# Performance work log

Measured on AMD Instinct MI355X. Metric: run time of the kernel, lower is better.

Reference implementation:

```python
import jax, jax.numpy as jnp
import numpy as np

NUM_HEADS = 16
ROPE_BASE = 10000.0


def _rope_interleaved(x, cos, sin):
    # x: [B,S,H,Hd]; cos/sin: [S,Hd/2]. Interleaved pairs (even, odd).
    x1 = x[..., 0::2]
    x2 = x[..., 1::2]
    c = cos[None, :, None, :]
    s = sin[None, :, None, :]
    o1 = x1 * c - x2 * s
    o2 = x1 * s + x2 * c
    return jnp.stack([o1, o2], axis=-1).reshape(x.shape)


def setup_inputs() -> dict:
    key = jax.random.key(0)
    ks = jax.random.split(key, 5)
    B, S, D = 2, 2048, 2048
    init_scale = 0.02
    x = jax.random.normal(ks[0], (B, S, D), jnp.float32)
    Wq = jax.random.normal(ks[1], (D, D), jnp.float32) * init_scale
    Wk = jax.random.normal(ks[2], (D, D), jnp.float32) * init_scale
    Wv = jax.random.normal(ks[3], (D, D), jnp.float32) * init_scale
    Wo = jax.random.normal(ks[4], (D, D), jnp.float32) * init_scale
    return {"x": x, "Wq": Wq, "Wk": Wk, "Wv": Wv, "Wo": Wo}


def reference(x, Wq, Wk, Wv, Wo):
    B, S, D = x.shape
    H = NUM_HEADS
    Hd = D // H
    # QKV projections (bias-free)
    q = (x @ Wq).reshape(B, S, H, Hd)
    k = (x @ Wk).reshape(B, S, H, Hd)
    v = (x @ Wv).reshape(B, S, H, Hd)
    # Rotary embedding, interleaved, base 10000, full head_dim
    pos = jnp.arange(S, dtype=jnp.float32)
    inv_freq = 1.0 / (ROPE_BASE ** (jnp.arange(0, Hd, 2, dtype=jnp.float32) / Hd))
    angles = pos[:, None] * inv_freq[None, :]  # [S, Hd/2]
    cos, sin = jnp.cos(angles), jnp.sin(angles)
    q = _rope_interleaved(q, cos, sin)
    k = _rope_interleaved(k, cos, sin)
    # Causal scaled-dot-product attention (flash_attn_func default scale = Hd**-0.5)
    scale = Hd ** -0.5
    scores = jnp.einsum('bqhd,bkhd->bhqk', q, k) * scale
    causal = jnp.tril(jnp.ones((S, S), dtype=bool))
    scores = jnp.where(causal[None, None], scores, jnp.finfo(scores.dtype).min)
    probs = jax.nn.softmax(scores, axis=-1)
    attn = jnp.einsum('bhqk,bkhd->bqhd', probs, v).reshape(B, S, D)
    return attn @ Wo
```

## Files before the change

### kernel.cpp

```cpp
#include <hip/hip_runtime.h>
#include <hip/hip_bf16.h>

static constexpr int BB = 2;
static constexpr int SS = 2048;
static constexpr int DD = 2048;
static constexpr int HH = 16;
static constexpr int HD = 128;

typedef __bf16 bf16_t;
typedef __bf16 bf16x8 __attribute__((ext_vector_type(8)));
typedef __bf16 bf16x4 __attribute__((ext_vector_type(4)));
typedef float  floatx4 __attribute__((ext_vector_type(4)));

__device__ __forceinline__ void gl2lds16(const bf16_t* g, bf16_t* l) {
    __builtin_amdgcn_global_load_lds(
        (const __attribute__((address_space(1))) void*)g,
        (__attribute__((address_space(3))) void*)l, 16, 0, 0);
}

__global__ void cast_x_kernel(const float* __restrict__ x, bf16_t* __restrict__ xb) {
    int i = blockIdx.x * 256 + threadIdx.x;
    float4 v = ((const float4*)x)[i];
    bf16x4 o;
    o.x = (bf16_t)v.x; o.y = (bf16_t)v.y; o.z = (bf16_t)v.z; o.w = (bf16_t)v.w;
    ((bf16x4*)xb)[i] = o;
}

__global__ void transpose_cast_kernel(const float* __restrict__ W, bf16_t* __restrict__ Wt) {
    __shared__ float tile[32][33];
    int bx = blockIdx.x * 32;
    int by = blockIdx.y * 32;
    int tx = threadIdx.x, ty = threadIdx.y;
#pragma unroll
    for (int j = 0; j < 4; ++j)
        tile[ty + j * 8][tx] = W[(size_t)(by + ty + j * 8) * DD + bx + tx];
    __syncthreads();
#pragma unroll
    for (int j = 0; j < 4; ++j)
        Wt[(size_t)(bx + ty + j * 8) * DD + by + tx] = (bf16_t)tile[tx][ty + j * 8];
}

template <int MODE>
__global__ __launch_bounds__(256, 2) void gemm_bt_kernel(
    const bf16_t* __restrict__ A, const bf16_t* __restrict__ Bt,
    float* __restrict__ Cf, bf16_t* __restrict__ Qw, bf16_t* __restrict__ Kw,
    bf16_t* __restrict__ Vw, int N, int K) {
    __shared__ __align__(16) bf16_t As[128 * 64];
    __shared__ __align__(16) bf16_t Bs[128 * 64];

    const int t = threadIdx.x;
    const int lane = t & 63;
    const int wave = t >> 6;
    const int lrow = lane & 15;
    const int lkq  = lane >> 4;
    const int wm = (wave & 1) * 64;
    const int wn = (wave >> 1) * 64;
    const int m0 = blockIdx.y * 128;
    const int n0 = blockIdx.x * 128;

    floatx4 acc[4][4];
#pragma unroll
    for (int i = 0; i < 4; ++i)
#pragma unroll
        for (int j = 0; j < 4; ++j) acc[i][j] = (floatx4)0.0f;

    const int srow  = lane >> 3;
    const int sch   = (lane & 7) ^ srow;

    for (int k0 = 0; k0 < K; k0 += 64) {
        __syncthreads();
#pragma unroll
        for (int p = 0; p < 4; ++p) {
            int r = wave * 32 + p * 8 + srow;
            gl2lds16(A  + (size_t)(m0 + r) * K + k0 + sch * 8, As + (wave * 32 + p * 8) * 64);
            gl2lds16(Bt + (size_t)(n0 + r) * K + k0 + sch * 8, Bs + (wave * 32 + p * 8) * 64);
        }
        __syncthreads();
#pragma unroll
        for (int ks = 0; ks < 2; ++ks) {
            bf16x8 af[4], bg[4];
#pragma unroll
            for (int i = 0; i < 4; ++i) {
                int pos = ((ks * 4 + lkq) ^ (lrow & 7)) * 8;
                af[i] = *(const bf16x8*)(As + (wm + i * 16 + lrow) * 64 + pos);
                bg[i] = *(const bf16x8*)(Bs + (wn + i * 16 + lrow) * 64 + pos);
            }
#pragma unroll
            for (int i = 0; i < 4; ++i)
#pragma unroll
                for (int j = 0; j < 4; ++j)
                    acc[i][j] = __builtin_amdgcn_mfma_f32_16x16x32_bf16(af[i], bg[j], acc[i][j], 0, 0, 0);
        }
    }

#pragma unroll
    for (int i = 0; i < 4; ++i)
#pragma unroll
        for (int j = 0; j < 4; ++j)
#pragma unroll
            for (int r = 0; r < 4; ++r) {
                int m = m0 + wm + i * 16 + lkq * 4 + r;
                int n = n0 + wn + j * 16 + lrow;
                float v = acc[i][j][r];
                if (MODE == 1) {
                    Cf[(size_t)m * N + n] = v;
                } else {
                    bf16_t bv = (bf16_t)v;
                    int b = m >> 11, s = m & (SS - 1);
                    int nn = n & (DD - 1);
                    int h = nn >> 7, d = nn & 127;
                    size_t off = (((size_t)b * HH + h) * SS + s) * HD + d;
                    if (n < DD)            Qw[off] = bv;
                    else if (n < 2 * DD)   Kw[off] = bv;
                    else                   Vw[off] = bv;
                }
            }
}

__global__ void rope_kernel(bf16_t* __restrict__ Qw, bf16_t* __restrict__ Kw) {
    int idx = blockIdx.x * 256 + threadIdx.x;
    int i  = idx & 63;
    int s  = (idx >> 6) & (SS - 1);
    int bh = idx >> 17;
    float inv = expf(-(float)(2 * i) * (9.210340371976184f / 128.0f));
    float ang = (float)s * inv;
    float c = cosf(ang), sn = sinf(ang);
    size_t base = ((size_t)bh * SS + s) * HD + 2 * i;
    float q1 = (float)Qw[base], q2 = (float)Qw[base + 1];
    Qw[base]     = (bf16_t)(q1 * c - q2 * sn);
    Qw[base + 1] = (bf16_t)(q1 * sn + q2 * c);
    float k1 = (float)Kw[base], k2 = (float)Kw[base + 1];
    Kw[base]     = (bf16_t)(k1 * c - k2 * sn);
    Kw[base + 1] = (bf16_t)(k1 * sn + k2 * c);
}

__global__ void vtrans_kernel(const bf16_t* __restrict__ Vw, bf16_t* __restrict__ Vt) {
    __shared__ unsigned short lds[64][65];
    const int t = threadIdx.x;
    const int s0 = blockIdx.x * 64, d0 = blockIdx.y * 64, bh = blockIdx.z;
    const bf16_t* src = Vw + ((size_t)bh * SS + s0) * HD + d0;
    bf16_t* dst = Vt + ((size_t)bh * HD + d0) * SS + s0;
#pragma unroll
    for (int p = 0; p < 2; ++p) {
        int c = p * 256 + t;
        int s = c >> 3, ch = c & 7;
        uint4 v = *(const uint4*)(src + (size_t)s * HD + ch * 8);
        const unsigned short* pv = (const unsigned short*)&v;
#pragma unroll
        for (int e = 0; e < 8; ++e) lds[ch * 8 + e][s] = pv[e];
    }
    __syncthreads();
    {
        int d = t >> 2, sb = (t & 3) * 16;
        uint4 o[2];
        unsigned short* po = (unsigned short*)o;
#pragma unroll
        for (int e = 0; e < 16; ++e) po[e] = lds[d][sb + e];
        *(uint4*)(dst + (size_t)d * SS + sb) = o[0];
        *(uint4*)(dst + (size_t)d * SS + sb + 8) = o[1];
    }
}

__global__ __launch_bounds__(256, 2) void flash_attn_kernel(
    const bf16_t* __restrict__ Qw, const bf16_t* __restrict__ Kw,
    const bf16_t* __restrict__ Vtw, bf16_t* __restrict__ Attn) {
    __shared__ __align__(16) bf16_t Ks[64 * 128];
    __shared__ __align__(16) bf16_t Vs[128 * 64];
    __shared__ __align__(16) bf16_t Ps[4][16 * 72];

    const int t = threadIdx.x;
    const int lane = t & 63;
    const int wave = t >> 6;
    const int lrow = lane & 15;
    const int lkq  = lane >> 4;
    const int bx = blockIdx.x;
    const int qtile = (bx & 1) ? (bx >> 1) : (15 - (bx >> 1));
    const int bh = blockIdx.y;
    const int q0 = qtile * 128;

    const bf16_t* Qbh = Qw + (size_t)bh * SS * HD;
    const bf16_t* Kbh = Kw + (size_t)bh * SS * HD;
    const bf16_t* Vbh = Vtw + (size_t)bh * HD * SS;

    const int qb[2] = { q0 + wave * 16, q0 + 64 + wave * 16 };

    const float qscale = 0.08838834764831845f * 1.4426950408889634f;
    bf16x8 qf[2][4];
#pragma unroll
    for (int qs = 0; qs < 2; ++qs)
#pragma unroll
        for (int kc4 = 0; kc4 < 4; ++kc4) {
            qf[qs][kc4] = *(const bf16x8*)(Qbh + (size_t)(qb[qs] + lrow) * HD + kc4 * 32 + lkq * 8);
#pragma unroll
            for (int e = 0; e < 8; ++e) qf[qs][kc4][e] = (bf16_t)((float)qf[qs][kc4][e] * qscale);
        }

    floatx4 oacc[2][8];
#pragma unroll
    for (int qs = 0; qs < 2; ++qs)
#pragma unroll
        for (int i = 0; i < 8; ++i) oacc[qs][i] = (floatx4)0.0f;
    float m_i[2] = { -1e30f, -1e30f };
    float l_i[2] = { 0.0f, 0.0f };

    const int nch = 2 * qtile + 2;
    for (int kc = 0; kc < nch; ++kc) {
        __syncthreads();
#pragma unroll
        for (int p = 0; p < 4; ++p) {
            int row = wave * 16 + p * 4 + (lane >> 4);
            int gch = (lane & 15) ^ (row & 7);
            gl2lds16(Kbh + (size_t)(kc * 64 + row) * HD + gch * 8,
                     Ks + (wave * 16 + p * 4) * 128);
        }
#pragma unroll
        for (int p = 0; p < 4; ++p) {
            int row = wave * 32 + p * 8 + (lane >> 3);
            int gch = (lane & 7) ^ (row & 7);
            gl2lds16(Vbh + (size_t)row * SS + kc * 64 + gch * 8,
                     Vs + (wave * 32 + p * 8) * 64);
        }
        __syncthreads();

        const bool act0 = (kc * 64 <= qb[0] + 15);

        floatx4 sacc[2][4];
#pragma unroll
        for (int qs = 0; qs < 2; ++qs)
#pragma unroll
            for (int i = 0; i < 4; ++i) sacc[qs][i] = (floatx4)0.0f;
#pragma unroll
        for (int nf = 0; nf < 4; ++nf)
#pragma unroll
            for (int kc4 = 0; kc4 < 4; ++kc4) {
                bf16x8 kf = *(const bf16x8*)(Ks + (nf * 16 + lrow) * 128 +
                                             (((kc4 * 4 + lkq) ^ (lrow & 7)) * 8));
                if (act0)
                    sacc[0][nf] = __builtin_amdgcn_mfma_f32_16x16x32_bf16(kf, qf[0][kc4], sacc[0][nf], 0, 0, 0);
                sacc[1][nf] = __builtin_amdgcn_mfma_f32_16x16x32_bf16(kf, qf[1][kc4], sacc[1][nf], 0, 0, 0);
            }

        bf16x8 pa[2][2];
#pragma unroll
        for (int qs = 0; qs < 2; ++qs) {
            const int qbase = qb[qs];
            if (qs == 0 && !act0) continue;

            const int qg = qbase + lrow;
            float mx = m_i[qs];
            if (kc * 64 + 63 > qbase) {
#pragma unroll
                for (int nf = 0; nf < 4; ++nf)
#pragma unroll
                    for (int r = 0; r < 4; ++r) {
                        int kg = kc * 64 + nf * 16 + lkq * 4 + r;
                        float sv = (kg > qg) ? -1e30f : sacc[qs][nf][r];
                        sacc[qs][nf][r] = sv;
                        mx = fmaxf(mx, sv);
                    }
            } else {
#pragma unroll
                for (int nf = 0; nf < 4; ++nf)
#pragma unroll
                    for (int r = 0; r < 4; ++r) mx = fmaxf(mx, sacc[qs][nf][r]);
            }
            mx = fmaxf(mx, __shfl_xor(mx, 16));
            mx = fmaxf(mx, __shfl_xor(mx, 32));
            float alpha = exp2f(m_i[qs] - mx);
            m_i[qs] = mx;

            float rs = 0.0f;
#pragma unroll
            for (int nf = 0; nf < 4; ++nf)
#pragma unroll
                for (int r = 0; r < 4; ++r) {
                    float pv = exp2f(sacc[qs][nf][r] - mx);
                    sacc[qs][nf][r] = pv;
                    rs += pv;
                }
            rs += __shfl_xor(rs, 16);
            rs += __shfl_xor(rs, 32);
            l_i[qs] = l_i[qs] * alpha + rs;

            if (__ballot(alpha < 1.0f)) {
                float av[4];
#pragma unroll
                for (int r = 0; r < 4; ++r) av[r] = __shfl(alpha, lkq * 4 + r);
#pragma unroll
                for (int nf8 = 0; nf8 < 8; ++nf8)
#pragma unroll
                    for (int r = 0; r < 4; ++r) oacc[qs][nf8][r] *= av[r];
            }

#pragma unroll
            for (int nf = 0; nf < 4; ++nf) {
                bf16x4 pk;
#pragma unroll
                for (int r = 0; r < 4; ++r) pk[r] = (bf16_t)sacc[qs][nf][r];
                *(bf16x4*)(Ps[wave] + lrow * 72 + nf * 16 + lkq * 4) = pk;
            }
#pragma unroll
            for (int k2 = 0; k2 < 2; ++k2)
                pa[qs][k2] = *(const bf16x8*)(Ps[wave] + lrow * 72 + k2 * 32 + lkq * 8);
        }

#pragma unroll
        for (int nf8 = 0; nf8 < 8; ++nf8)
#pragma unroll
            for (int k2 = 0; k2 < 2; ++k2) {
                bf16x8 vf = *(const bf16x8*)(Vs + (nf8 * 16 + lrow) * 64 +
                                             (((k2 * 4 + lkq) ^ (lrow & 7)) * 8));
                if (act0)
                    oacc[0][nf8] = __builtin_amdgcn_mfma_f32_16x16x32_bf16(pa[0][k2], vf, oacc[0][nf8], 0, 0, 0);
                oacc[1][nf8] = __builtin_amdgcn_mfma_f32_16x16x32_bf16(pa[1][k2], vf, oacc[1][nf8], 0, 0, 0);
            }
    }

    int bb = bh >> 4, h = bh & 15;
#pragma unroll
    for (int qs = 0; qs < 2; ++qs)
#pragma unroll
        for (int r = 0; r < 4; ++r) {
            float invl = 1.0f / __shfl(l_i[qs], lkq * 4 + r);
            int q = qb[qs] + lkq * 4 + r;
#pragma unroll
            for (int nf8 = 0; nf8 < 8; ++nf8)
                Attn[((size_t)bb * SS + q) * DD + h * HD + nf8 * 16 + lrow] =
                    (bf16_t)(oacc[qs][nf8][r] * invl);
        }
}

extern "C" void kernel_launch(void* const* d_in, const int* in_sizes, int n_in,
                              void* d_out, int out_size, void* d_ws, size_t ws_size,
                              hipStream_t stream) {
    const float* x  = (const float*)d_in[0];
    const float* Wq = (const float*)d_in[1];
    const float* Wk = (const float*)d_in[2];
    const float* Wv = (const float*)d_in[3];
    const float* Wo = (const float*)d_in[4];
    float* out = (float*)d_out;

    bf16_t* p = (bf16_t*)d_ws;
    bf16_t* Xb    = p; p += (size_t)BB * SS * DD;
    bf16_t* Wqkvt = p; p += (size_t)3 * DD * DD;
    bf16_t* Wot   = p; p += (size_t)DD * DD;
    bf16_t* Qw    = p; p += (size_t)BB * HH * SS * HD;
    bf16_t* Kw    = p; p += (size_t)BB * HH * SS * HD;
    bf16_t* Vtw   = p; p += (size_t)BB * HH * SS * HD;
    bf16_t* Attn  = p; p += (size_t)BB * SS * DD;
    bf16_t* Vw = Attn;

    cast_x_kernel<<<(BB * SS * DD / 4) / 256, 256, 0, stream>>>(x, Xb);

    dim3 tb(32, 8), tg(DD / 32, DD / 32);
    transpose_cast_kernel<<<tg, tb, 0, stream>>>(Wq, Wqkvt);
    transpose_cast_kernel<<<tg, tb, 0, stream>>>(Wk, Wqkvt + (size_t)DD * DD);
    transpose_cast_kernel<<<tg, tb, 0, stream>>>(Wv, Wqkvt + (size_t)2 * DD * DD);
    transpose_cast_kernel<<<tg, tb, 0, stream>>>(Wo, Wot);

    gemm_bt_kernel<0><<<dim3(3 * DD / 128, BB * SS / 128), 256, 0, stream>>>(
        Xb, Wqkvt, nullptr, Qw, Kw, Vw, 3 * DD, DD);

    rope_kernel<<<(BB * HH * SS * 64) / 256, 256, 0, stream>>>(Qw, Kw);

    vtrans_kernel<<<dim3(SS / 64, HD / 64, BB * HH), 256, 0, stream>>>(Vw, Vtw);

    flash_attn_kernel<<<dim3(SS / 128, BB * HH), 256, 0, stream>>>(Qw, Kw, Vtw, Attn);

    gemm_bt_kernel<1><<<dim3(DD / 128, BB * SS / 128), 256, 0, stream>>>(
        Attn, Wot, out, nullptr, nullptr, nullptr, DD, DD);
}
```

Measured before the change: 411.0 us.

## Split causal flash attention over KV chunks with a separate combine kernel

Each query tile's KV range is split into up to four segments of 8 chunks, one block per segment. Each block writes its unnormalized bf16 output and per-row max and sum to workspace, and a new combine kernel merges the partials with log-sum-exp rescaling. The aim is to shorten the critical path of the longest causal tiles and put more blocks on the many CUs. In exchange it adds extra global traffic, a second launch, more workspace, and some rounding from storing partials in bf16.

Result: slower. 455.2 us (+10.8%).

```diff
diff --git a/kernel.cpp b/kernel.cpp
--- a/kernel.cpp
+++ b/kernel.cpp
@@ -163,7 +163,8 @@
 
 __global__ __launch_bounds__(256, 2) void flash_attn_kernel(
     const bf16_t* __restrict__ Qw, const bf16_t* __restrict__ Kw,
-    const bf16_t* __restrict__ Vtw, bf16_t* __restrict__ Attn) {
+    const bf16_t* __restrict__ Vtw, bf16_t* __restrict__ Op,
+    float* __restrict__ mpart, float* __restrict__ lpart) {
     __shared__ __align__(16) bf16_t Ks[64 * 128];
     __shared__ __align__(16) bf16_t Vs[128 * 64];
     __shared__ __align__(16) bf16_t Ps[4][16 * 72];
@@ -173,10 +174,15 @@
     const int wave = t >> 6;
     const int lrow = lane & 15;
     const int lkq  = lane >> 4;
-    const int bx = blockIdx.x;
-    const int qtile = (bx & 1) ? (bx >> 1) : (15 - (bx >> 1));
+    const int qt = blockIdx.x >> 2;
+    const int sp = blockIdx.x & 3;
     const int bh = blockIdx.y;
-    const int q0 = qtile * 128;
+
+    const int nch = 2 * qt + 2;
+    const int kc0 = sp * 8;
+    if (kc0 >= nch) return;
+    const int kc1 = (kc0 + 8 < nch) ? kc0 + 8 : nch;
+    const int q0 = qt * 128;
 
     const bf16_t* Qbh = Qw + (size_t)bh * SS * HD;
     const bf16_t* Kbh = Kw + (size_t)bh * SS * HD;
@@ -203,8 +209,7 @@
     float m_i[2] = { -1e30f, -1e30f };
     float l_i[2] = { 0.0f, 0.0f };
 
-    const int nch = 2 * qtile + 2;
-    for (int kc = 0; kc < nch; ++kc) {
+    for (int kc = kc0; kc < kc1; ++kc) {
         __syncthreads();
 #pragma unroll
         for (int p = 0; p < 4; ++p) {
@@ -316,18 +321,59 @@
             }
     }
 
-    int bb = bh >> 4, h = bh & 15;
-#pragma unroll
-    for (int qs = 0; qs < 2; ++qs)
+    const int slot = (bh * 16 + qt) * 4 + sp;
+    bf16_t* Os = Op + (size_t)slot * (128 * 128);
+#pragma unroll
+    for (int qs = 0; qs < 2; ++qs) {
 #pragma unroll
         for (int r = 0; r < 4; ++r) {
-            float invl = 1.0f / __shfl(l_i[qs], lkq * 4 + r);
-            int q = qb[qs] + lkq * 4 + r;
+            int row = qs * 64 + wave * 16 + lkq * 4 + r;
 #pragma unroll
             for (int nf8 = 0; nf8 < 8; ++nf8)
-                Attn[((size_t)bb * SS + q) * DD + h * HD + nf8 * 16 + lrow] =
-                    (bf16_t)(oacc[qs][nf8][r] * invl);
-        }
+                Os[row * 128 + nf8 * 16 + lrow] = (bf16_t)oacc[qs][nf8][r];
+        }
+        if (lkq == 0) {
+            int row = qs * 64 + wave * 16 + lrow;
+            mpart[(size_t)slot * 128 + row] = m_i[qs];
+            lpart[(size_t)slot * 128 + row] = l_i[qs];
+        }
+    }
+}
+
+__global__ void combine_kernel(const bf16_t* __restrict__ Op,
+                               const float* __restrict__ mpart,
+                               const float* __restrict__ lpart,
+                               bf16_t* __restrict__ Attn) {
+    const int t = threadIdx.x;
+    const int qt = blockIdx.x;
+    const int bh = blockIdx.y;
+    const int ns = (qt >> 2) + 1;
+    const int slot0 = (bh * 16 + qt) * 4;
+    const int bb = bh >> 4, h = bh & 15;
+
+#pragma unroll 1
+    for (int rr = 0; rr < 8; ++rr) {
+        int q = rr * 16 + (t >> 4);
+        int dbase = (t & 15) * 8;
+        float M = -1e30f;
+        for (int s = 0; s < ns; ++s)
+            M = fmaxf(M, mpart[(size_t)(slot0 + s) * 128 + q]);
+        float l = 0.0f, acc[8];
+#pragma unroll
+        for (int e = 0; e < 8; ++e) acc[e] = 0.0f;
+        for (int s = 0; s < ns; ++s) {
+            float w = exp2f(mpart[(size_t)(slot0 + s) * 128 + q] - M);
+            l += w * lpart[(size_t)(slot0 + s) * 128 + q];
+            bf16x8 o = *(const bf16x8*)(Op + (size_t)(slot0 + s) * (128 * 128) + q * 128 + dbase);
+#pragma unroll
+            for (int e = 0; e < 8; ++e) acc[e] += w * (float)o[e];
+        }
+        float invl = 1.0f / l;
+        bf16x8 out;
+#pragma unroll
+        for (int e = 0; e < 8; ++e) out[e] = (bf16_t)(acc[e] * invl);
+        *(bf16x8*)(Attn + ((size_t)bb * SS + qt * 128 + q) * DD + h * HD + dbase) = out;
+    }
 }
 
 extern "C" void kernel_launch(void* const* d_in, const int* in_sizes, int n_in,
@@ -348,6 +394,9 @@
     bf16_t* Kw    = p; p += (size_t)BB * HH * SS * HD;
     bf16_t* Vtw   = p; p += (size_t)BB * HH * SS * HD;
     bf16_t* Attn  = p; p += (size_t)BB * SS * DD;
+    bf16_t* Op    = p; p += (size_t)2048 * 128 * 128;
+    float*  mpart = (float*)p;
+    float*  lpart = mpart + (size_t)2048 * 128;
     bf16_t* Vw = Attn;
 
     cast_x_kernel<<<(BB * SS * DD / 4) / 256, 256, 0, stream>>>(x, Xb);
@@ -365,7 +414,10 @@
 
     vtrans_kernel<<<dim3(SS / 64, HD / 64, BB * HH), 256, 0, stream>>>(Vw, Vtw);
 
-    flash_attn_kernel<<<dim3(SS / 128, BB * HH), 256, 0, stream>>>(Qw, Kw, Vtw, Attn);
+    flash_attn_kernel<<<dim3(16 * 4, BB * HH), 256, 0, stream>>>(
+        Qw, Kw, Vtw, Op, mpart, lpart);
+
+    combine_kernel<<<dim3(16, BB * HH), 256, 0, stream>>>(Op, mpart, lpart, Attn);
 
     gemm_bt_kernel<1><<<dim3(DD / 128, BB * SS / 128), 256, 0, stream>>>(
         Attn, Wot, out, nullptr, nullptr, nullptr, DD, DD);
```
